# Optimization experiments

Measured on AMD Instinct MI355X. Metric: run time of the kernel, lower is better.

## Reference

```python
import jax, jax.numpy as jnp
import numpy as np
from jax import lax

B, CIN, COUT, H, W, K = 16, 256, 384, 56, 56, 3
HOUT = H - K + 1  # 54, valid conv
MAP_RADIUS = (COUT - 1) // 2  # 191
LFB_SIGMA = float(MAP_RADIUS)  # default lfb_sigma = map_radius.max()


def _lfb_kernel():
    # Gaussian lateral-feedback kernel over the 1D channel map (lfb_gauss)
    d = jnp.abs(jnp.arange(COUT, dtype=jnp.float32) - MAP_RADIUS)
    return jnp.exp(-(d ** 2) / (2.0 * LFB_SIGMA ** 2))


def setup_inputs() -> dict:
    key = jax.random.key(0)
    k1, k2 = jax.random.split(key)
    x = jax.random.normal(k1, (B, CIN, H, W), dtype=jnp.float32)
    stdv = 1.0 / np.sqrt(CIN * K * K)
    weight = jax.random.uniform(k2, (COUT, CIN, K, K), dtype=jnp.float32,
                                minval=-stdv, maxval=stdv)
    return {"x": x, "weight": weight}


def reference(x, weight):
    # out_sim = kernel_mult2d: plain valid conv2d, stride 1
    y = lax.conv_general_dilated(x, weight, window_strides=(1, 1), padding='VALID',
                                 dimension_numbers=('NCHW', 'OIHW', 'NCHW'))  # (B,COUT,54,54)
    # Competitive operates on (N, out_channels): flatten batch+spatial, channel-last
    yf = y.transpose(0, 2, 3, 1).reshape(-1, COUT)  # (N, C)
    # winner-take-all, k=1: binary mask of per-row max (non-differentiable, like torch compare)
    mx = jnp.max(yf, axis=1, keepdims=True)
    winner_mask = lax.stop_gradient((yf >= mx).astype(yf.dtype))
    # lateral feedback: pad channel map and conv1d with Gaussian kernel
    pad_pre = MAP_RADIUS
    pad_post = COUT - 1 - MAP_RADIUS
    lfb_in = jnp.pad(winner_mask, ((0, 0), (pad_pre, pad_post)))[:, None, :]  # (N,1,2C-1)
    kern = _lfb_kernel()[None, None, :]  # (1,1,C)
    lfb_out = lax.conv_general_dilated(lfb_in, kern, window_strides=(1,), padding='VALID',
                                       dimension_numbers=('NCH', 'OIH', 'NCH'))[:, 0, :]  # (N,C)
    lfb_out = jnp.clip(lfb_out, -1.0, 1.0)
    # lfb_y_gating: gate lateral-feedback output by activations
    out = lfb_out * yf
    return out.reshape(B, HOUT, HOUT, COUT).transpose(0, 3, 1, 2)
```

## Files before the change

### kernel.cpp

```cpp
#include <hip/hip_runtime.h>

#define CIN   256
#define COUT  384
#define HH    56
#define WW    56
#define HO    54
#define NB    16
#define NPIX  (NB*HO*HO)
#define KK    (CIN*9)
#define XCH   (HH*WW)
#define XIMG  (CIN*HH*WW)

#define BM 128
#define BN 128
#define NCHUNK (KK/32)
#define KGRP   (KK/8)
#define WPLANE (KGRP*COUT*8)

#define WS_OFF_OFF (6u << 20)
#define WS_Y_OFF   (8u << 20)

typedef __bf16  bf16x8 __attribute__((ext_vector_type(8)));
typedef float   f32x16 __attribute__((ext_vector_type(16)));
typedef ushort  us8    __attribute__((ext_vector_type(8)));

__device__ __forceinline__ ushort rne_bf16(float f) {
    unsigned u = __float_as_uint(f);
    return (ushort)((u + 0x7FFFu + ((u >> 16) & 1u)) >> 16);
}
__device__ __forceinline__ void split3(float v, ushort& h1, ushort& h2, ushort& h3) {
    h1 = rne_bf16(v);
    float r1 = v - __uint_as_float((unsigned)h1 << 16);
    h2 = rne_bf16(r1);
    float r2 = r1 - __uint_as_float((unsigned)h2 << 16);
    h3 = rne_bf16(r2);
}

__global__ __launch_bounds__(256) void wsplit(const float* __restrict__ w,
                                              ushort* __restrict__ wg) {
    int idx = blockIdx.x * 256 + threadIdx.x;
    int cout = idx / KK, k = idx - cout * KK;
    ushort h1, h2, h3;
    split3(w[idx], h1, h2, h3);
    int base = ((k >> 3) * COUT + cout) * 8 + (k & 7);
    wg[base]              = h1;
    wg[WPLANE + base]     = h2;
    wg[2 * WPLANE + base] = h3;
}

__global__ __launch_bounds__(256) void offk_init(int* __restrict__ offg) {
    int k = blockIdx.x * 256 + threadIdx.x;
    if (k < KK) {
        int cin = k / 9, r = k - cin * 9;
        int dy = r / 3, dx = r - dy * 3;
        offg[k] = cin * XCH + dy * WW + dx;
    }
}

__global__ __launch_bounds__(256, 3) void conv_mfma(const float* __restrict__ x,
                                                    const ushort* __restrict__ wg,
                                                    const int* __restrict__ offg,
                                                    float* __restrict__ y) {
    __shared__ __align__(16) ushort As[3][4][128][8];
    __shared__ __align__(16) ushort Bs[3][4][128][8];

    const int tid = threadIdx.x;
    const int c0 = blockIdx.y * BM;
    const int p0 = blockIdx.x * BN;

    const int nb  = tid & 127;
    const int gb0 = tid >> 7;
    int pbase;
    {
        int p = p0 + nb; if (p >= NPIX) p = NPIX - 1;
        int b = p / 2916, rem = p - b * 2916;
        int oy = rem / 54, ox = rem - oy * 54;
        pbase = b * XIMG + oy * WW + ox;
    }

    const int lane = tid & 63;
    const int wv = tid >> 6;
    const int wr = wv >> 1, wc = wv & 1;
    const int l31 = lane & 31, lg = lane >> 5;
    const int mrow = wr * 64 + l31;
    const int ncol = wc * 64 + l31;

    f32x16 acc[2][2];
#pragma unroll
    for (int i = 0; i < 2; ++i)
#pragma unroll
        for (int j = 0; j < 2; ++j) acc[i][j] = (f32x16)0.f;

    float4 aPre[6];
    float  bPre[2][8];
    us8    bSpl[2][3];

    auto PREFETCH = [&](int c) {
#pragma unroll
        for (int r = 0; r < 6; ++r) {
            int flat = r * 256 + tid;
            int s = flat >> 9;
            int g = (flat >> 7) & 3;
            int m = flat & 127;
            aPre[r] = *(const float4*)(wg + ((s * KGRP + (c * 4 + g)) * COUT + (c0 + m)) * 8);
        }
#pragma unroll
        for (int t = 0; t < 2; ++t) {
            int kb = c * 32 + (gb0 + 2 * t) * 8;
            int4 o0 = *(const int4*)(offg + kb);
            int4 o1 = *(const int4*)(offg + kb + 4);
            bPre[t][0] = x[pbase + o0.x];
            bPre[t][1] = x[pbase + o0.y];
            bPre[t][2] = x[pbase + o0.z];
            bPre[t][3] = x[pbase + o0.w];
            bPre[t][4] = x[pbase + o1.x];
            bPre[t][5] = x[pbase + o1.y];
            bPre[t][6] = x[pbase + o1.z];
            bPre[t][7] = x[pbase + o1.w];
        }
    };

    auto SPLITB = [&]() {
#pragma unroll
        for (int t = 0; t < 2; ++t) {
            us8 h1v, h2v, h3v;
#pragma unroll
            for (int kk = 0; kk < 8; ++kk) {
                ushort a, b, c2;
                split3(bPre[t][kk], a, b, c2);
                h1v[kk] = a; h2v[kk] = b; h3v[kk] = c2;
            }
            bSpl[t][0] = h1v; bSpl[t][1] = h2v; bSpl[t][2] = h3v;
        }
    };

    auto WRITE = [&]() {
#pragma unroll
        for (int r = 0; r < 6; ++r) {
            int flat = r * 256 + tid;
            *(float4*)((ushort*)As + flat * 8) = aPre[r];
        }
#pragma unroll
        for (int t = 0; t < 2; ++t) {
            int g = gb0 + 2 * t;
#pragma unroll
            for (int s = 0; s < 3; ++s)
                *(us8*)&Bs[s][g][nb][0] = bSpl[t][s];
        }
    };

    auto COMPUTE = [&]() {
        bf16x8 af[3][2][2];
#pragma unroll
        for (int s = 0; s < 3; ++s)
#pragma unroll
            for (int mi = 0; mi < 2; ++mi)
#pragma unroll
                for (int ks = 0; ks < 2; ++ks)
                    af[s][mi][ks] = *(const bf16x8*)&As[s][2 * ks + lg][mrow + mi * 32][0];
#pragma unroll
        for (int sb = 0; sb < 3; ++sb) {
            bf16x8 bf[2][2];
#pragma unroll
            for (int ni = 0; ni < 2; ++ni)
#pragma unroll
                for (int ks = 0; ks < 2; ++ks)
                    bf[ni][ks] = *(const bf16x8*)&Bs[sb][2 * ks + lg][ncol + ni * 32][0];
#pragma unroll
            for (int sa = 0; sa + sb < 3; ++sa)
#pragma unroll
                for (int ks = 0; ks < 2; ++ks)
#pragma unroll
                    for (int mi = 0; mi < 2; ++mi)
#pragma unroll
                        for (int ni = 0; ni < 2; ++ni)
                            acc[mi][ni] = __builtin_amdgcn_mfma_f32_32x32x16_bf16(
                                af[sa][mi][ks], bf[ni][ks], acc[mi][ni], 0, 0, 0);
        }
    };

    PREFETCH(0);
    SPLITB();
    WRITE();
    __syncthreads();

    for (int c = 0; ; ) {
        if (c + 1 < NCHUNK) { PREFETCH(c + 1); SPLITB(); }
        COMPUTE();
        if (++c == NCHUNK) break;
        __syncthreads();
        WRITE();
        __syncthreads();
    }

#pragma unroll
    for (int ni = 0; ni < 2; ++ni) {
        int col = p0 + wc * 64 + ni * 32 + l31;
        if (col < NPIX) {
#pragma unroll
            for (int mi = 0; mi < 2; ++mi) {
                int rb = c0 + wr * 64 + mi * 32 + 4 * lg;
#pragma unroll
                for (int reg = 0; reg < 16; ++reg) {
                    int row = rb + (reg & 3) + 8 * (reg >> 2);
                    y[row * NPIX + col] = acc[mi][ni][reg];
                }
            }
        }
    }
}

__global__ __launch_bounds__(256) void gate(const float* __restrict__ y,
                                            float* __restrict__ out) {
    __shared__ float ys[COUT][33];
    __shared__ float gtab[COUT];
    __shared__ float pmax[8][32];
    __shared__ float mx[32];
    __shared__ int   wcnt[32];
    __shared__ int   wlist[32][4];

    const int tid = threadIdx.x;
    const int tx = tid & 31, ty = tid >> 5;
    const int p0 = blockIdx.x * 32;

    for (int k = tid; k < COUT; k += 256) {
        float d = (float)(k - 191);
        gtab[k] = expf(-d * d * (1.0f / (2.0f * 191.0f * 191.0f)));
    }
    if (ty == 0) wcnt[tx] = 0;

    for (int c = ty; c < COUT; c += 8)
        ys[c][tx] = y[c * NPIX + p0 + tx];
    __syncthreads();

    float m = -3.402823466e+38f;
    for (int c = ty; c < COUT; c += 8) m = fmaxf(m, ys[c][tx]);
    pmax[ty][tx] = m;
    __syncthreads();
    if (ty == 0) {
        float mm = pmax[0][tx];
#pragma unroll
        for (int r = 1; r < 8; ++r) mm = fmaxf(mm, pmax[r][tx]);
        mx[tx] = mm;
    }
    __syncthreads();

    const float mm = mx[tx];
    for (int c = ty; c < COUT; c += 8) {
        if (ys[c][tx] >= mm) {
            int pos = atomicAdd(&wcnt[tx], 1);
            if (pos < 4) wlist[tx][pos] = c;
        }
    }
    __syncthreads();

    const int p   = p0 + tx;
    const int b   = p / 2916;
    const int rem = p - b * 2916;
    const int obase = b * (COUT * 2916) + rem;
    const int L = min(wcnt[tx], 4);
    for (int c = ty; c < COUT; c += 8) {
        float lfb = 0.f;
        for (int i = 0; i < L; ++i) {
            int d = wlist[tx][i] - c + 191;
            if (d >= 0 && d < COUT) lfb += gtab[d];
        }
        lfb = fminf(lfb, 1.0f);
        out[obase + c * 2916] = lfb * ys[c][tx];
    }
}

extern "C" void kernel_launch(void* const* d_in, const int* in_sizes, int n_in,
                              void* d_out, int out_size, void* d_ws, size_t ws_size,
                              hipStream_t stream) {
    const float* x = (const float*)d_in[0];
    const float* w = (const float*)d_in[1];
    float* outp = (float*)d_out;

    ushort* wg   = (ushort*)d_ws;
    int*    offg = (int*)((char*)d_ws + WS_OFF_OFF);
    float*  y    = (float*)((char*)d_ws + WS_Y_OFF);

    wsplit<<<(KK * COUT) / 256, 256, 0, stream>>>(w, wg);
    offk_init<<<(KK + 255) / 256, 256, 0, stream>>>(offg);

    dim3 grid((NPIX + BN - 1) / BN, COUT / BM);
    conv_mfma<<<grid, 256, 0, stream>>>(x, wg, offg, y);

    gate<<<NPIX / 32, 256, 0, stream>>>(y, outp);
}
```

Baseline: 995.7 us.

## Double-buffer LDS with K=16 chunks and a single barrier per iteration

```diff
diff --git a/kernel.cpp b/kernel.cpp
--- a/kernel.cpp
+++ b/kernel.cpp
@@ -13,7 +13,7 @@
 
 #define BM 128
 #define BN 128
-#define NCHUNK (KK/32)
+#define NCHUNK (KK/16)
 #define KGRP   (KK/8)
 #define WPLANE (KGRP*COUT*8)
 
@@ -61,15 +61,15 @@
                                                     const ushort* __restrict__ wg,
                                                     const int* __restrict__ offg,
                                                     float* __restrict__ y) {
-    __shared__ __align__(16) ushort As[3][4][128][8];
-    __shared__ __align__(16) ushort Bs[3][4][128][8];
+    __shared__ __align__(16) ushort As[2][3][2][128][8];
+    __shared__ __align__(16) ushort Bs[2][3][2][128][8];
 
     const int tid = threadIdx.x;
     const int c0 = blockIdx.y * BM;
     const int p0 = blockIdx.x * BN;
 
-    const int nb  = tid & 127;
-    const int gb0 = tid >> 7;
+    const int nb = tid & 127;
+    const int gb = tid >> 7;
     int pbase;
     {
         int p = p0 + nb; if (p >= NPIX) p = NPIX - 1;
@@ -82,8 +82,8 @@
     const int wv = tid >> 6;
     const int wr = wv >> 1, wc = wv & 1;
     const int l31 = lane & 31, lg = lane >> 5;
-    const int mrow = wr * 64 + l31;
-    const int ncol = wc * 64 + l31;
+    const int arow = wr * 64 + l31;
+    const int brow = wc * 64 + l31;
 
     f32x16 acc[2][2];
 #pragma unroll
@@ -91,106 +91,76 @@
 #pragma unroll
         for (int j = 0; j < 2; ++j) acc[i][j] = (f32x16)0.f;
 
-    float4 aPre[6];
-    float  bPre[2][8];
-    us8    bSpl[2][3];
+    float4 aPre[3];
+    float  bPre[8];
 
     auto PREFETCH = [&](int c) {
-#pragma unroll
-        for (int r = 0; r < 6; ++r) {
-            int flat = r * 256 + tid;
-            int s = flat >> 9;
-            int g = (flat >> 7) & 3;
-            int m = flat & 127;
-            aPre[r] = *(const float4*)(wg + ((s * KGRP + (c * 4 + g)) * COUT + (c0 + m)) * 8);
-        }
-#pragma unroll
-        for (int t = 0; t < 2; ++t) {
-            int kb = c * 32 + (gb0 + 2 * t) * 8;
-            int4 o0 = *(const int4*)(offg + kb);
-            int4 o1 = *(const int4*)(offg + kb + 4);
-            bPre[t][0] = x[pbase + o0.x];
-            bPre[t][1] = x[pbase + o0.y];
-            bPre[t][2] = x[pbase + o0.z];
-            bPre[t][3] = x[pbase + o0.w];
-            bPre[t][4] = x[pbase + o1.x];
-            bPre[t][5] = x[pbase + o1.y];
-            bPre[t][6] = x[pbase + o1.z];
-            bPre[t][7] = x[pbase + o1.w];
-        }
+        const ushort* wp = wg + ((2 * c + gb) * COUT + c0 + nb) * 8;
+#pragma unroll
+        for (int r = 0; r < 3; ++r)
+            aPre[r] = *(const float4*)(wp + r * WPLANE);
+        int kb = c * 16 + gb * 8;
+        int4 o0 = *(const int4*)(offg + kb);
+        int4 o1 = *(const int4*)(offg + kb + 4);
+        bPre[0] = x[pbase + o0.x];
+        bPre[1] = x[pbase + o0.y];
+        bPre[2] = x[pbase + o0.z];
+        bPre[3] = x[pbase + o0.w];
+        bPre[4] = x[pbase + o1.x];
+        bPre[5] = x[pbase + o1.y];
+        bPre[6] = x[pbase + o1.z];
+        bPre[7] = x[pbase + o1.w];
     };
 
-    auto SPLITB = [&]() {
-#pragma unroll
-        for (int t = 0; t < 2; ++t) {
-            us8 h1v, h2v, h3v;
-#pragma unroll
-            for (int kk = 0; kk < 8; ++kk) {
-                ushort a, b, c2;
-                split3(bPre[t][kk], a, b, c2);
-                h1v[kk] = a; h2v[kk] = b; h3v[kk] = c2;
+    auto WRITE = [&](int buf) {
+#pragma unroll
+        for (int r = 0; r < 3; ++r)
+            *(float4*)&As[buf][r][gb][nb][0] = aPre[r];
+        us8 h1v, h2v, h3v;
+#pragma unroll
+        for (int kk = 0; kk < 8; ++kk) {
+            ushort a, b, c2;
+            split3(bPre[kk], a, b, c2);
+            h1v[kk] = a; h2v[kk] = b; h3v[kk] = c2;
+        }
+        *(us8*)&Bs[buf][0][gb][nb][0] = h1v;
+        *(us8*)&Bs[buf][1][gb][nb][0] = h2v;
+        *(us8*)&Bs[buf][2][gb][nb][0] = h3v;
+    };
+
+    auto COMPUTE = [&](int buf) {
+        bf16x8 af[3][2];
+#pragma unroll
+        for (int s = 0; s < 3; ++s)
+#pragma unroll
+            for (int mi = 0; mi < 2; ++mi)
+                af[s][mi] = *(const bf16x8*)&As[buf][s][lg][arow + mi * 32][0];
+#pragma unroll
+        for (int sb = 0; sb < 3; ++sb) {
+            bf16x8 bf0 = *(const bf16x8*)&Bs[buf][sb][lg][brow][0];
+            bf16x8 bf1 = *(const bf16x8*)&Bs[buf][sb][lg][brow + 32][0];
+#pragma unroll
+            for (int sa = 0; sa + sb < 3; ++sa) {
+                acc[0][0] = __builtin_amdgcn_mfma_f32_32x32x16_bf16(af[sa][0], bf0, acc[0][0], 0, 0, 0);
+                acc[0][1] = __builtin_amdgcn_mfma_f32_32x32x16_bf16(af[sa][0], bf1, acc[0][1], 0, 0, 0);
+                acc[1][0] = __builtin_amdgcn_mfma_f32_32x32x16_bf16(af[sa][1], bf0, acc[1][0], 0, 0, 0);
+                acc[1][1] = __builtin_amdgcn_mfma_f32_32x32x16_bf16(af[sa][1], bf1, acc[1][1], 0, 0, 0);
             }
-            bSpl[t][0] = h1v; bSpl[t][1] = h2v; bSpl[t][2] = h3v;
         }
     };
 
-    auto WRITE = [&]() {
-#pragma unroll
-        for (int r = 0; r < 6; ++r) {
-            int flat = r * 256 + tid;
-            *(float4*)((ushort*)As + flat * 8) = aPre[r];
-        }
-#pragma unroll
-        for (int t = 0; t < 2; ++t) {
-            int g = gb0 + 2 * t;
-#pragma unroll
-            for (int s = 0; s < 3; ++s)
-                *(us8*)&Bs[s][g][nb][0] = bSpl[t][s];
-        }
-    };
-
-    auto COMPUTE = [&]() {
-        bf16x8 af[3][2][2];
-#pragma unroll
-        for (int s = 0; s < 3; ++s)
-#pragma unroll
-            for (int mi = 0; mi < 2; ++mi)
-#pragma unroll
-                for (int ks = 0; ks < 2; ++ks)
-                    af[s][mi][ks] = *(const bf16x8*)&As[s][2 * ks + lg][mrow + mi * 32][0];
-#pragma unroll
-        for (int sb = 0; sb < 3; ++sb) {
-            bf16x8 bf[2][2];
-#pragma unroll
-            for (int ni = 0; ni < 2; ++ni)
-#pragma unroll
-                for (int ks = 0; ks < 2; ++ks)
-                    bf[ni][ks] = *(const bf16x8*)&Bs[sb][2 * ks + lg][ncol + ni * 32][0];
-#pragma unroll
-            for (int sa = 0; sa + sb < 3; ++sa)
-#pragma unroll
-                for (int ks = 0; ks < 2; ++ks)
-#pragma unroll
-                    for (int mi = 0; mi < 2; ++mi)
-#pragma unroll
-                        for (int ni = 0; ni < 2; ++ni)
-                            acc[mi][ni] = __builtin_amdgcn_mfma_f32_32x32x16_bf16(
-                                af[sa][mi][ks], bf[ni][ks], acc[mi][ni], 0, 0, 0);
-        }
-    };
-
     PREFETCH(0);
-    SPLITB();
-    WRITE();
-    __syncthreads();
-
+    WRITE(0);
+    __syncthreads();
+
+    int cur = 0;
     for (int c = 0; ; ) {
-        if (c + 1 < NCHUNK) { PREFETCH(c + 1); SPLITB(); }
-        COMPUTE();
+        if (c + 1 < NCHUNK) PREFETCH(c + 1);
+        COMPUTE(cur);
         if (++c == NCHUNK) break;
+        WRITE(cur ^ 1);
         __syncthreads();
-        WRITE();
-        __syncthreads();
+        cur ^= 1;
     }
 
 #pragma unroll
```

Result: faster. 892.6 us (-10.4%).
